# Optimization experiments

Hardware: AMD Instinct MI355X
Metric: run time of the kernel (lower is better)

## Reference

```python
import jax, jax.numpy as jnp
import numpy as np


def setup_inputs() -> dict:
    key = jax.random.key(0)
    k1, k2, k3 = jax.random.split(key, 3)
    B, C, H, W = 16, 256, 80, 80
    MED, K = 128, 128
    x = jax.random.normal(k1, (B, C, H, W), dtype=jnp.float32)
    w1 = jax.random.normal(k2, (MED, C), dtype=jnp.float32) * 0.05
    b1 = jnp.zeros((MED,), dtype=jnp.float32)
    w2 = jax.random.normal(k3, (C, MED), dtype=jnp.float32) * 0.05
    b2 = jnp.zeros((C,), dtype=jnp.float32)
    return {"x": x, "w1": w1, "b1": b1, "w2": w2, "b2": b2, "out_c": K}


def reference(x, w1, b1, w2, b2, out_c):
    # 1x1 conv MLP: in_c -> med_c -> in_c (pointwise GEMMs)
    h = jnp.einsum('bchw,mc->bmhw', x, w1) + b1[None, :, None, None]
    x_ = jnp.einsum('bmhw,cm->bchw', h, w2) + b2[None, :, None, None]
    xs = jax.nn.sigmoid(x_)
    # per-pixel top-k over channels: work in NHWC so channel is last axis
    xs_t = jnp.transpose(xs, (0, 2, 3, 1))              # [B,H,W,C]
    _, xi = jax.lax.top_k(xs_t, out_c)                  # [B,H,W,K]
    x_t = jnp.transpose(x, (0, 2, 3, 1))                # [B,H,W,C]
    xl_t = jnp.transpose(x_, (0, 2, 3, 1))              # [B,H,W,C]
    out1 = jnp.take_along_axis(x_t, xi, axis=-1)        # [B,H,W,K]
    out2 = jnp.take_along_axis(xl_t, xi, axis=-1)       # [B,H,W,K]
    return jnp.transpose(out1 * out2, (0, 3, 1, 2))     # [B,K,H,W]
```

## Files before the change

### kernel.cpp

```cpp
#include <hip/hip_runtime.h>
#include <math.h>

#define CIN  256
#define MEDC 128
#define KOUT 128
#define HWSZ 6400
#define NB   16
#define TP   16
#define SROW 272

typedef unsigned int u32;
typedef unsigned long long u64;

__device__ __forceinline__ float numpy_expf(float x) {
#pragma clang fp contract(off)
    const float q = __builtin_rintf(x * 1.44269504088896341f);
    float r = __builtin_fmaf(q, -0.693359375f, x);
    r = __builtin_fmaf(q, 2.12194440e-4f, r);
    float p = __builtin_fmaf(1.9875691500e-4f, r, 1.3981999507e-3f);
    p = __builtin_fmaf(p, r, 8.3334519073e-3f);
    p = __builtin_fmaf(p, r, 4.1665795894e-2f);
    p = __builtin_fmaf(p, r, 1.6666665459e-1f);
    p = __builtin_fmaf(p, r, 5.0000001201e-1f);
    const float r2 = r * r;
    p = __builtin_fmaf(p, r2, r);
    p = p + 1.0f;
    return __builtin_ldexpf(p, (int)q);
}

__global__ void prep_T(const float* __restrict__ w1, const float* __restrict__ w2,
                       float* __restrict__ w1t, float* __restrict__ w2t) {
    const int c = blockIdx.x;
    const int m = threadIdx.x;
    w1t[c * MEDC + m] = w1[m * CIN + c];
    const int q  = c & 63;
    const int ci = c >> 6;
    w2t[m * CIN + q * 4 + ci] = w2[c * MEDC + m];
}


template<int D, int STAGE>
__device__ __forceinline__ void intra_ct(u64 (&k)[16]) {
#pragma unroll
    for (int r = 0; r < 16; ++r) {
        if (!(r & D)) {
            const bool dsc = (r >> STAGE) & 1;
            const bool sw  = (k[r] > k[r ^ D]) != dsc;
            const u64 x0 = k[r], x1 = k[r ^ D];
            k[r]     = sw ? x1 : x0;
            k[r ^ D] = sw ? x0 : x1;
        }
    }
}

template<int D>
__device__ __forceinline__ void intra_rt(u64 (&k)[16], const bool dsc) {
#pragma unroll
    for (int r = 0; r < 16; ++r) {
        if (!(r & D)) {
            const bool sw = (k[r] > k[r ^ D]) != dsc;
            const u64 x0 = k[r], x1 = k[r ^ D];
            k[r]     = sw ? x1 : x0;
            k[r ^ D] = sw ? x0 : x1;
        }
    }
}

template<int SWZ>
__device__ __forceinline__ u64 swz64(u64 v) {
    const int lo = __builtin_amdgcn_ds_swizzle((int)(unsigned)v, SWZ);
    const int hi = __builtin_amdgcn_ds_swizzle((int)(unsigned)(v >> 32), SWZ);
    return ((u64)(unsigned)hi << 32) | (u64)(unsigned)lo;
}

template<int M, int SWZ>
__device__ __forceinline__ void cross_rt(u64 (&k)[16], const int l16, const bool dsc) {
    const bool keepmax = ((l16 & M) != 0) != dsc;
#pragma unroll
    for (int r = 0; r < 16; ++r) {
        const u64 other = swz64<SWZ>(k[r]);
        const bool gt = k[r] > other;
        k[r] = (gt == keepmax) ? k[r] : other;
    }
}

__global__ __launch_bounds__(256, 4)
void csel_main(const float* __restrict__ x,
               const float* __restrict__ w1t, const float* __restrict__ w2t,
               const float* __restrict__ b1, const float* __restrict__ b2,
               float* __restrict__ out) {
    __shared__ __align__(16) float xs[CIN * 20];
    __shared__ __align__(16) u32 s_arr[TP * SROW];

    const int t    = threadIdx.x;
    const int pix0 = blockIdx.x * TP;
    const int b    = pix0 / HWSZ;
    const int hw0  = pix0 % HWSZ;
    const float* xb = x + (size_t)b * CIN * HWSZ + hw0;

    {
        const int p  = t & (TP - 1);
        const int c0 = t >> 4;
        #pragma unroll
        for (int i = 0; i < 16; ++i) {
            const int c = c0 + i * 16;
            xs[c * 20 + p] = xb[(size_t)c * HWSZ + p];
        }
    }
    __syncthreads();

    const int lw = t & 63;
    const int wq = t >> 6;
    const int ml = lw * 2;
    const float b1a = b1[ml];
    const float b1b = b1[ml + 1];
    float a1[2][4] = {{0.f,0.f,0.f,0.f},{0.f,0.f,0.f,0.f}};

    #pragma unroll 4
    for (int c = 0; c < CIN; ++c) {
        const float2 wv = *(const float2*)&w1t[c * MEDC + ml];
        const float4 xv = *(const float4*)&xs[c * 20 + wq * 4];
        a1[0][0] = fmaf(wv.x, xv.x, a1[0][0]);
        a1[0][1] = fmaf(wv.x, xv.y, a1[0][1]);
        a1[0][2] = fmaf(wv.x, xv.z, a1[0][2]);
        a1[0][3] = fmaf(wv.x, xv.w, a1[0][3]);
        a1[1][0] = fmaf(wv.y, xv.x, a1[1][0]);
        a1[1][1] = fmaf(wv.y, xv.y, a1[1][1]);
        a1[1][2] = fmaf(wv.y, xv.z, a1[1][2]);
        a1[1][3] = fmaf(wv.y, xv.w, a1[1][3]);
    }
    float h8[8];
    #pragma unroll
    for (int j = 0; j < 4; ++j) {
        h8[j]     = a1[0][j] + b1a;
        h8[4 + j] = a1[1][j] + b1b;
    }

    const float b2v0 = b2[lw];
    const float b2v1 = b2[lw + 64];
    const float b2v2 = b2[lw + 128];
    const float b2v3 = b2[lw + 192];
    const float* w2p = w2t + lw * 4;

    float4 wbuf[8];
    #pragma unroll
    for (int m0 = 0; m0 < 8; ++m0)
        wbuf[m0] = *(const float4*)&w2p[m0 * CIN];

    float a2[4][4];
    #pragma unroll
    for (int i = 0; i < 4; ++i)
        #pragma unroll
        for (int j = 0; j < 4; ++j) a2[i][j] = 0.f;

    #pragma unroll
    for (int m = 0; m < MEDC; ++m) {
        const float4 wv = wbuf[m & 7];
        float hb[4];
        #pragma unroll
        for (int pj = 0; pj < 4; ++pj) {
            const int reg = (m & 1) * 4 + pj;
            hb[pj] = __int_as_float(
                __builtin_amdgcn_readlane(__float_as_int(h8[reg]), m >> 1));
        }
        a2[0][0] = fmaf(wv.x, hb[0], a2[0][0]);
        a2[0][1] = fmaf(wv.x, hb[1], a2[0][1]);
        a2[0][2] = fmaf(wv.x, hb[2], a2[0][2]);
        a2[0][3] = fmaf(wv.x, hb[3], a2[0][3]);
        a2[1][0] = fmaf(wv.y, hb[0], a2[1][0]);
        a2[1][1] = fmaf(wv.y, hb[1], a2[1][1]);
        a2[1][2] = fmaf(wv.y, hb[2], a2[1][2]);
        a2[1][3] = fmaf(wv.y, hb[3], a2[1][3]);
        a2[2][0] = fmaf(wv.z, hb[0], a2[2][0]);
        a2[2][1] = fmaf(wv.z, hb[1], a2[2][1]);
        a2[2][2] = fmaf(wv.z, hb[2], a2[2][2]);
        a2[2][3] = fmaf(wv.z, hb[3], a2[2][3]);
        a2[3][0] = fmaf(wv.w, hb[0], a2[3][0]);
        a2[3][1] = fmaf(wv.w, hb[1], a2[3][1]);
        a2[3][2] = fmaf(wv.w, hb[2], a2[3][2]);
        a2[3][3] = fmaf(wv.w, hb[3], a2[3][3]);
        if (m + 8 < MEDC)
            wbuf[m & 7] = *(const float4*)&w2p[(m + 8) * CIN];
    }
    float xv32[4][4];
    #pragma unroll
    for (int pj = 0; pj < 4; ++pj) {
        xv32[0][pj] = a2[0][pj] + b2v0;
        xv32[1][pj] = a2[1][pj] + b2v1;
        xv32[2][pj] = a2[2][pj] + b2v2;
        xv32[3][pj] = a2[3][pj] + b2v3;
    }
    __syncthreads();

    #pragma unroll
    for (int ci = 0; ci < 4; ++ci) {
        const int c    = lw + 64 * ci;
        const int slot = c + (c >> 4);
        #pragma unroll
        for (int pj = 0; pj < 4; ++pj) {
#pragma clang fp contract(off)
            const int p2 = wq * 4 + pj;
            const float e  = numpy_expf(-xv32[ci][pj]);
            const float dd = 1.0f + e;
            const float s  = 1.0f / dd;
            s_arr[p2 * SROW + slot] = __float_as_uint(s);
            xs[c * 20 + p2] = xs[c * 20 + p2] * xv32[ci][pj];
        }
    }
    __syncthreads();

    const int p   = t >> 4;
    const int l16 = t & 15;

    u64 k[16];
    {
        const u32* sp = &s_arr[p * SROW + l16 * 17];
        const int cbase = l16 * 16;
        #pragma unroll
        for (int r = 0; r < 16; ++r) {
            const u64 s = (u64)sp[r];
            k[r] = (s << 8) | (u64)(255 - (cbase + r));
        }
    }

    intra_ct<1, 1>(k);
    intra_ct<2, 2>(k); intra_ct<1, 2>(k);
    intra_ct<4, 3>(k); intra_ct<2, 3>(k); intra_ct<1, 3>(k);
    {
        const bool dsc = (l16 & 1) != 0;
        intra_rt<8>(k, dsc); intra_rt<4>(k, dsc); intra_rt<2>(k, dsc); intra_rt<1>(k, dsc);
    }
    {
        const bool dsc = ((l16 >> 1) & 1) != 0;
        cross_rt<1, 0x041F>(k, l16, dsc);
        intra_rt<8>(k, dsc); intra_rt<4>(k, dsc); intra_rt<2>(k, dsc); intra_rt<1>(k, dsc);
    }
    {
        const bool dsc = ((l16 >> 2) & 1) != 0;
        cross_rt<2, 0x081F>(k, l16, dsc);
        cross_rt<1, 0x041F>(k, l16, dsc);
        intra_rt<8>(k, dsc); intra_rt<4>(k, dsc); intra_rt<2>(k, dsc); intra_rt<1>(k, dsc);
    }
    {
        const bool dsc = ((l16 >> 3) & 1) != 0;
        cross_rt<4, 0x101F>(k, l16, dsc);
        cross_rt<2, 0x081F>(k, l16, dsc);
        cross_rt<1, 0x041F>(k, l16, dsc);
        intra_rt<8>(k, dsc); intra_rt<4>(k, dsc); intra_rt<2>(k, dsc); intra_rt<1>(k, dsc);
    }
    {
        cross_rt<8, 0x201F>(k, l16, false);
        cross_rt<4, 0x101F>(k, l16, false);
        cross_rt<2, 0x081F>(k, l16, false);
        cross_rt<1, 0x041F>(k, l16, false);
        intra_rt<8>(k, false); intra_rt<4>(k, false); intra_rt<2>(k, false); intra_rt<1>(k, false);
    }

    if (l16 >= 8) {
        const int rbase = 255 - l16 * 16;
        float* ob = out + (size_t)b * KOUT * HWSZ + hw0 + p;
        #pragma unroll
        for (int r = 0; r < 16; ++r) {
            const int c = 255 - (int)(k[r] & 0xFF);
            ob[(size_t)(rbase - r) * HWSZ] = xs[c * 20 + p];
        }
    }
}

extern "C" void kernel_launch(void* const* d_in, const int* in_sizes, int n_in,
                              void* d_out, int out_size, void* d_ws, size_t ws_size,
                              hipStream_t stream) {
    const float* x  = (const float*)d_in[0];
    const float* w1 = (const float*)d_in[1];
    const float* b1 = (const float*)d_in[2];
    const float* w2 = (const float*)d_in[3];
    const float* b2 = (const float*)d_in[4];

    float* w1t = (float*)d_ws;
    float* w2t = w1t + CIN * MEDC;

    prep_T<<<CIN, MEDC, 0, stream>>>(w1, w2, w1t, w2t);
    csel_main<<<(NB * HWSZ) / TP, 256, 0, stream>>>(x, w1t, w2t, b1, b2, (float*)d_out);
}
```

Baseline: 504.0 us.

## Sort keys as doubles with fmin/fmax, shuffle scores in registers, raise occupancy

The top-k bitonic sort now reinterprets the packed 64-bit keys as doubles, so each compare-exchange is a single fmin/fmax pair instead of integer compares and selects. It uses flip-style merges, so no per-lane direction flags are needed. Sigmoid scores are redistributed through ds_swizzle and shfl_xor in registers instead of a shared-memory staging array, which removes that LDS buffer. The weight prefetch depth drops from 8 to 4 and launch bounds rise to 8 blocks per CU, trading register-level prefetch for occupancy. This relies on the positive-float-derived keys ordering correctly when read as doubles, and the higher occupancy target may force register spills.

```diff
diff --git a/kernel.cpp b/kernel.cpp
--- a/kernel.cpp
+++ b/kernel.cpp
@@ -7,7 +7,6 @@
 #define HWSZ 6400
 #define NB   16
 #define TP   16
-#define SROW 272
 
 typedef unsigned int u32;
 typedef unsigned long long u64;
@@ -39,58 +38,58 @@
 }
 
 
-template<int D, int STAGE>
-__device__ __forceinline__ void intra_ct(u64 (&k)[16]) {
+template<int MASK>
+__device__ __forceinline__ void intraX(double (&k)[16]) {
 #pragma unroll
     for (int r = 0; r < 16; ++r) {
-        if (!(r & D)) {
-            const bool dsc = (r >> STAGE) & 1;
-            const bool sw  = (k[r] > k[r ^ D]) != dsc;
-            const u64 x0 = k[r], x1 = k[r ^ D];
-            k[r]     = sw ? x1 : x0;
-            k[r ^ D] = sw ? x0 : x1;
-        }
-    }
-}
-
-template<int D>
-__device__ __forceinline__ void intra_rt(u64 (&k)[16], const bool dsc) {
+        if (r < (r ^ MASK)) {
+            const double a = k[r], bb = k[r ^ MASK];
+            k[r]        = fmin(a, bb);
+            k[r ^ MASK] = fmax(a, bb);
+        }
+    }
+}
+
+template<int SWZ>
+__device__ __forceinline__ double swzd(double v) {
+    const u64 x = (u64)__double_as_longlong(v);
+    const int lo = __builtin_amdgcn_ds_swizzle((int)(u32)x, SWZ);
+    const int hi = __builtin_amdgcn_ds_swizzle((int)(u32)(x >> 32), SWZ);
+    return __longlong_as_double((long long)(((u64)(u32)hi << 32) | (u64)(u32)lo));
+}
+
+template<int SWZ, int UB>
+__device__ __forceinline__ void crossFlip(double (&k)[16], const int u) {
+    const bool keepmin = (u & UB) == 0;
+#pragma unroll
+    for (int r = 0; r < 8; ++r) {
+        const int q = r ^ 15;
+        const double o1 = swzd<SWZ>(k[q]);
+        const double o2 = swzd<SWZ>(k[r]);
+        const double mn1 = fmin(k[r], o1), mx1 = fmax(k[r], o1);
+        const double mn2 = fmin(k[q], o2), mx2 = fmax(k[q], o2);
+        k[r] = keepmin ? mn1 : mx1;
+        k[q] = keepmin ? mn2 : mx2;
+    }
+}
+
+template<int SWZ, int UB>
+__device__ __forceinline__ void crossU(double (&k)[16], const int u) {
+    const bool keepmin = (u & UB) == 0;
 #pragma unroll
     for (int r = 0; r < 16; ++r) {
-        if (!(r & D)) {
-            const bool sw = (k[r] > k[r ^ D]) != dsc;
-            const u64 x0 = k[r], x1 = k[r ^ D];
-            k[r]     = sw ? x1 : x0;
-            k[r ^ D] = sw ? x0 : x1;
-        }
-    }
-}
-
-template<int SWZ>
-__device__ __forceinline__ u64 swz64(u64 v) {
-    const int lo = __builtin_amdgcn_ds_swizzle((int)(unsigned)v, SWZ);
-    const int hi = __builtin_amdgcn_ds_swizzle((int)(unsigned)(v >> 32), SWZ);
-    return ((u64)(unsigned)hi << 32) | (u64)(unsigned)lo;
-}
-
-template<int M, int SWZ>
-__device__ __forceinline__ void cross_rt(u64 (&k)[16], const int l16, const bool dsc) {
-    const bool keepmax = ((l16 & M) != 0) != dsc;
-#pragma unroll
-    for (int r = 0; r < 16; ++r) {
-        const u64 other = swz64<SWZ>(k[r]);
-        const bool gt = k[r] > other;
-        k[r] = (gt == keepmax) ? k[r] : other;
-    }
-}
-
-__global__ __launch_bounds__(256, 4)
+        const double o = swzd<SWZ>(k[r]);
+        const double mn = fmin(k[r], o), mx = fmax(k[r], o);
+        k[r] = keepmin ? mn : mx;
+    }
+}
+
+__global__ __launch_bounds__(256, 8)
 void csel_main(const float* __restrict__ x,
                const float* __restrict__ w1t, const float* __restrict__ w2t,
                const float* __restrict__ b1, const float* __restrict__ b2,
                float* __restrict__ out) {
     __shared__ __align__(16) float xs[CIN * 20];
-    __shared__ __align__(16) u32 s_arr[TP * SROW];
 
     const int t    = threadIdx.x;
     const int pix0 = blockIdx.x * TP;
@@ -142,9 +141,9 @@
     const float b2v3 = b2[lw + 192];
     const float* w2p = w2t + lw * 4;
 
-    float4 wbuf[8];
-    #pragma unroll
-    for (int m0 = 0; m0 < 8; ++m0)
+    float4 wbuf[4];
+    #pragma unroll
+    for (int m0 = 0; m0 < 4; ++m0)
         wbuf[m0] = *(const float4*)&w2p[m0 * CIN];
 
     float a2[4][4];
@@ -155,7 +154,7 @@
 
     #pragma unroll
     for (int m = 0; m < MEDC; ++m) {
-        const float4 wv = wbuf[m & 7];
+        const float4 wv = wbuf[m & 3];
         float hb[4];
         #pragma unroll
         for (int pj = 0; pj < 4; ++pj) {
@@ -179,8 +178,8 @@
         a2[3][1] = fmaf(wv.w, hb[1], a2[3][1]);
         a2[3][2] = fmaf(wv.w, hb[2], a2[3][2]);
         a2[3][3] = fmaf(wv.w, hb[3], a2[3][3]);
-        if (m + 8 < MEDC)
-            wbuf[m & 7] = *(const float4*)&w2p[(m + 8) * CIN];
+        if (m + 4 < MEDC)
+            wbuf[m & 3] = *(const float4*)&w2p[(m + 4) * CIN];
     }
     float xv32[4][4];
     #pragma unroll
@@ -192,10 +191,10 @@
     }
     __syncthreads();
 
+    u32 sv[4][4];
     #pragma unroll
     for (int ci = 0; ci < 4; ++ci) {
-        const int c    = lw + 64 * ci;
-        const int slot = c + (c >> 4);
+        const int c = lw + 64 * ci;
         #pragma unroll
         for (int pj = 0; pj < 4; ++pj) {
 #pragma clang fp contract(off)
@@ -203,65 +202,71 @@
             const float e  = numpy_expf(-xv32[ci][pj]);
             const float dd = 1.0f + e;
             const float s  = 1.0f / dd;
-            s_arr[p2 * SROW + slot] = __float_as_uint(s);
+            sv[ci][pj] = __float_as_uint(s);
             xs[c * 20 + p2] = xs[c * 20 + p2] * xv32[ci][pj];
         }
     }
     __syncthreads();
 
-    const int p   = t >> 4;
-    const int l16 = t & 15;
-
-    u64 k[16];
-    {
-        const u32* sp = &s_arr[p * SROW + l16 * 17];
-        const int cbase = l16 * 16;
+    const int a0 = (t >> 4) & 1;
+    const int a1b = (t >> 5) & 1;
+    #pragma unroll
+    for (int ci = 0; ci < 4; ++ci) {
+        {
+            const u32 s0 = (u32)__builtin_amdgcn_ds_swizzle((int)sv[ci][1], 0x401F);
+            const u32 s1 = (u32)__builtin_amdgcn_ds_swizzle((int)sv[ci][0], 0x401F);
+            const u32 s2 = (u32)__builtin_amdgcn_ds_swizzle((int)sv[ci][3], 0x401F);
+            const u32 s3 = (u32)__builtin_amdgcn_ds_swizzle((int)sv[ci][2], 0x401F);
+            sv[ci][0] = a0 ? s0 : sv[ci][0];
+            sv[ci][1] = a0 ? sv[ci][1] : s1;
+            sv[ci][2] = a0 ? s2 : sv[ci][2];
+            sv[ci][3] = a0 ? sv[ci][3] : s3;
+        }
+        {
+            const u32 s0 = (u32)__shfl_xor((int)sv[ci][2], 32, 64);
+            const u32 s1 = (u32)__shfl_xor((int)sv[ci][3], 32, 64);
+            const u32 s2 = (u32)__shfl_xor((int)sv[ci][0], 32, 64);
+            const u32 s3 = (u32)__shfl_xor((int)sv[ci][1], 32, 64);
+            sv[ci][0] = a1b ? s0 : sv[ci][0];
+            sv[ci][1] = a1b ? s1 : sv[ci][1];
+            sv[ci][2] = a1b ? sv[ci][2] : s2;
+            sv[ci][3] = a1b ? sv[ci][3] : s3;
+        }
+    }
+
+    const int u = t & 15;
+    double k[16];
+    #pragma unroll
+    for (int ci = 0; ci < 4; ++ci) {
+        #pragma unroll
+        for (int bb = 0; bb < 4; ++bb) {
+            const int r = bb + 4 * ci;
+            const u64 key = ((u64)sv[ci][bb] << 8) | (u64)(255 - (u + 16 * r));
+            k[r] = __longlong_as_double((long long)key);
+        }
+    }
+
+    intraX<1>(k);
+    intraX<3>(k); intraX<1>(k);
+    intraX<7>(k); intraX<2>(k); intraX<1>(k);
+    intraX<15>(k); intraX<4>(k); intraX<2>(k); intraX<1>(k);
+    crossFlip<0x041F,1>(k,u);
+    intraX<8>(k); intraX<4>(k); intraX<2>(k); intraX<1>(k);
+    crossFlip<0x0C1F,2>(k,u); crossU<0x041F,1>(k,u);
+    intraX<8>(k); intraX<4>(k); intraX<2>(k); intraX<1>(k);
+    crossFlip<0x1C1F,4>(k,u); crossU<0x081F,2>(k,u); crossU<0x041F,1>(k,u);
+    intraX<8>(k); intraX<4>(k); intraX<2>(k); intraX<1>(k);
+    crossFlip<0x3C1F,8>(k,u); crossU<0x101F,4>(k,u); crossU<0x081F,2>(k,u); crossU<0x041F,1>(k,u);
+    intraX<8>(k); intraX<4>(k); intraX<2>(k); intraX<1>(k);
+
+    const int p = t >> 4;
+    if (u >= 8) {
+        const int rbase = 255 - u * 16;
+        float* ob = out + (size_t)b * KOUT * HWSZ + hw0 + p;
         #pragma unroll
         for (int r = 0; r < 16; ++r) {
-            const u64 s = (u64)sp[r];
-            k[r] = (s << 8) | (u64)(255 - (cbase + r));
-        }
-    }
-
-    intra_ct<1, 1>(k);
-    intra_ct<2, 2>(k); intra_ct<1, 2>(k);
-    intra_ct<4, 3>(k); intra_ct<2, 3>(k); intra_ct<1, 3>(k);
-    {
-        const bool dsc = (l16 & 1) != 0;
-        intra_rt<8>(k, dsc); intra_rt<4>(k, dsc); intra_rt<2>(k, dsc); intra_rt<1>(k, dsc);
-    }
-    {
-        const bool dsc = ((l16 >> 1) & 1) != 0;
-        cross_rt<1, 0x041F>(k, l16, dsc);
-        intra_rt<8>(k, dsc); intra_rt<4>(k, dsc); intra_rt<2>(k, dsc); intra_rt<1>(k, dsc);
-    }
-    {
-        const bool dsc = ((l16 >> 2) & 1) != 0;
-        cross_rt<2, 0x081F>(k, l16, dsc);
-        cross_rt<1, 0x041F>(k, l16, dsc);
-        intra_rt<8>(k, dsc); intra_rt<4>(k, dsc); intra_rt<2>(k, dsc); intra_rt<1>(k, dsc);
-    }
-    {
-        const bool dsc = ((l16 >> 3) & 1) != 0;
-        cross_rt<4, 0x101F>(k, l16, dsc);
-        cross_rt<2, 0x081F>(k, l16, dsc);
-        cross_rt<1, 0x041F>(k, l16, dsc);
-        intra_rt<8>(k, dsc); intra_rt<4>(k, dsc); intra_rt<2>(k, dsc); intra_rt<1>(k, dsc);
-    }
-    {
-        cross_rt<8, 0x201F>(k, l16, false);
-        cross_rt<4, 0x101F>(k, l16, false);
-        cross_rt<2, 0x081F>(k, l16, false);
-        cross_rt<1, 0x041F>(k, l16, false);
-        intra_rt<8>(k, false); intra_rt<4>(k, false); intra_rt<2>(k, false); intra_rt<1>(k, false);
-    }
-
-    if (l16 >= 8) {
-        const int rbase = 255 - l16 * 16;
-        float* ob = out + (size_t)b * KOUT * HWSZ + hw0 + p;
-        #pragma unroll
-        for (int r = 0; r < 16; ++r) {
-            const int c = 255 - (int)(k[r] & 0xFF);
+            const u64 kb = (u64)__double_as_longlong(k[r]);
+            const int c = 255 - (int)(kb & 0xFF);
             ob[(size_t)(rbase - r) * HWSZ] = xs[c * 20 + p];
         }
     }
```

After: 987.9 us. 96.0% more time.
